# Kernel tuning notes

Measured on AMD Instinct MI355X. Metric: run time of the kernel, lower is better.

## Reference

```python
import jax, jax.numpy as jnp
import numpy as np

E = 8          # num_experts
TOP_K = 2      # router top-k
ALPHA = 1.702  # swigluoai alpha
LIMIT = 7.0    # swigluoai clamp limit


def setup_inputs() -> dict:
    key = jax.random.key(0)
    ks = jax.random.split(key, 7)
    B, S, H, I = 2, 1024, 1024, 1024
    s = 1.0 / np.sqrt(H)  # keep activations O(1), realistic init scale
    return {
        "x": jax.random.normal(ks[0], (B, S, H), jnp.float32),
        "router_weight": jax.random.normal(ks[1], (E, H), jnp.float32) * s,
        "router_bias": jax.random.normal(ks[2], (E,), jnp.float32) * 0.01,
        "w1": jax.random.normal(ks[3], (E, H, 2 * I), jnp.float32) * s,  # interleaved gate/up
        "w1_bias": jax.random.normal(ks[4], (E, 2 * I), jnp.float32) * 0.01,
        "w2": jax.random.normal(ks[5], (E, I, H), jnp.float32) * s,
        "w2_bias": jax.random.normal(ks[6], (E, H), jnp.float32) * 0.01,
    }


def _moe(x, router_weight, router_bias, w1, w1_bias, w2, w2_bias):
    B, S, H = x.shape
    xf = x.reshape(-1, H)                                   # [T, H]
    # ---- router: softmax over expert logits, then top-k ----
    logits = xf @ router_weight.T + router_bias             # [T, E]
    probs = jax.nn.softmax(logits, axis=-1)
    expert_weights, expert_ids = jax.lax.top_k(probs, TOP_K)  # [T, k]
    # combine weights scattered to dense [T, E] (no normalization: normalize_expert_weights=None)
    combine = jnp.sum(jax.nn.one_hot(expert_ids, E, dtype=xf.dtype)
                      * expert_weights[..., None], axis=1)  # [T, E]
    # ---- grouped MLP, expressed densely per expert (reference semantics) ----
    h = jnp.einsum('th,ehi->eti', xf, w1) + w1_bias[:, None, :]   # [E, T, 2I]
    gate = h[..., 0::2]                                          # interleaved layout
    up = h[..., 1::2]
    gate = jnp.minimum(gate, LIMIT)                              # swigluoai: clamp gate max
    up = jnp.clip(up, -LIMIT, LIMIT)                             # clamp up both sides
    glu = gate * jax.nn.sigmoid(gate * ALPHA)
    act = (up + 1.0) * glu                                       # [E, T, I]
    y = jnp.einsum('eti,eih->eth', act, w2) + w2_bias[:, None, :]  # [E, T, H]
    out = jnp.einsum('eth,te->th', y, combine)                   # weighted combine
    return out.reshape(B, S, H), expert_weights


def reference(x, router_weight, router_bias, w1, w1_bias, w2, w2_bias):
    return _moe(x, router_weight, router_bias, w1, w1_bias, w2, w2_bias)
```

## Files before the change

kernel.cpp:

```cpp
#include <hip/hip_runtime.h>
#include <cstdint>
#include <cstddef>

typedef unsigned short u16;
typedef short bf16x8 __attribute__((ext_vector_type(8)));
typedef float floatx4 __attribute__((ext_vector_type(4)));

#define GLD16(gp, sp) __builtin_amdgcn_global_load_lds(                      \
    (const __attribute__((address_space(1))) void*)(gp),                     \
    (__attribute__((address_space(3))) void*)(sp), 16, 0, 0)

#define VWAIT(N) asm volatile("s_waitcnt vmcnt(" #N ")" ::: "memory")
#define BARF()                                                               \
  do {                                                                       \
    __builtin_amdgcn_sched_barrier(0);                                       \
    __builtin_amdgcn_s_barrier();                                            \
    __builtin_amdgcn_sched_barrier(0);                                       \
  } while (0)

__device__ __forceinline__ u16 f2bf(float f) {
  unsigned u = __float_as_uint(f);
  u += 0x7fffu + ((u >> 16) & 1u);
  return (u16)(u >> 16);
}

__global__ void transpose_cvt_kernel(const float* __restrict__ in, u16* __restrict__ out,
                                     int R, int C) {
  __shared__ float tile[32][33];
  size_t base = (size_t)blockIdx.z * (size_t)R * (size_t)C;
  int c0 = blockIdx.x * 32, r0 = blockIdx.y * 32;
  int tx = threadIdx.x, ty = threadIdx.y;
#pragma unroll
  for (int k = 0; k < 32; k += 8)
    tile[ty + k][tx] = in[base + (size_t)(r0 + ty + k) * C + (c0 + tx)];
  __syncthreads();
#pragma unroll
  for (int k = 0; k < 32; k += 8)
    out[base + (size_t)(c0 + ty + k) * R + (r0 + tx)] = f2bf(tile[tx][ty + k]);
}

__global__ void router_kernel(const float* __restrict__ x, const float* __restrict__ rw,
                              const float* __restrict__ rb, float* __restrict__ ew,
                              int* __restrict__ eids, float* __restrict__ eprobs,
                              u16* __restrict__ xb) {
  const int wave = threadIdx.x >> 6, lane = threadIdx.x & 63;
  const int t = blockIdx.x * 4 + wave;
  const float4* xv = (const float4*)(x + (size_t)t * 1024);
  ushort4* xo = (ushort4*)(xb + (size_t)t * 1024);
  float acc[8];
#pragma unroll
  for (int e = 0; e < 8; ++e) acc[e] = 0.f;
  for (int j = lane; j < 256; j += 64) {
    float4 xx = xv[j];
    ushort4 o;
    o.x = f2bf(xx.x); o.y = f2bf(xx.y); o.z = f2bf(xx.z); o.w = f2bf(xx.w);
    xo[j] = o;
#pragma unroll
    for (int e = 0; e < 8; ++e) {
      float4 wv = ((const float4*)(rw + (size_t)e * 1024))[j];
      acc[e] += xx.x * wv.x + xx.y * wv.y + xx.z * wv.z + xx.w * wv.w;
    }
  }
#pragma unroll
  for (int e = 0; e < 8; ++e) {
    float v = acc[e];
#pragma unroll
    for (int off = 32; off > 0; off >>= 1) v += __shfl_down(v, off);
    acc[e] = v;
  }
  if (lane == 0) {
    float p[8];
    float mx = -1e30f;
#pragma unroll
    for (int e = 0; e < 8; ++e) { p[e] = acc[e] + rb[e]; mx = fmaxf(mx, p[e]); }
    float sum = 0.f;
#pragma unroll
    for (int e = 0; e < 8; ++e) { p[e] = __expf(p[e] - mx); sum += p[e]; }
    float inv = 1.f / sum;
#pragma unroll
    for (int e = 0; e < 8; ++e) p[e] *= inv;
    int i0 = 0;
#pragma unroll
    for (int e = 1; e < 8; ++e) if (p[e] > p[i0]) i0 = e;
    int i1 = (i0 == 0) ? 1 : 0;
#pragma unroll
    for (int e = 0; e < 8; ++e) if (e != i0 && e != i1 && p[e] > p[i1]) i1 = e;
    ew[t * 2 + 0] = p[i0];
    ew[t * 2 + 1] = p[i1];
    eids[t * 2 + 0] = i0;
    eids[t * 2 + 1] = i1;
    eprobs[t * 2 + 0] = p[i0];
    eprobs[t * 2 + 1] = p[i1];
  }
}

__global__ void build_lists_kernel(const int* __restrict__ eids, const float* __restrict__ eprobs,
                                   int* __restrict__ row_token, float* __restrict__ row_scale,
                                   int* __restrict__ tok2slot, int* __restrict__ meta) {
  __shared__ int cnt[8], base[8], cur[8];
  const int tid = threadIdx.x;
  if (tid < 8) { cnt[tid] = 0; cur[tid] = 0; }
  __syncthreads();
  for (int t = tid; t < 2048; t += 256) {
    atomicAdd(&cnt[eids[t * 2 + 0]], 1);
    atomicAdd(&cnt[eids[t * 2 + 1]], 1);
  }
  __syncthreads();
  if (tid == 0) {
    int off = 0, w = 0;
    for (int e = 0; e < 8; ++e) {
      base[e] = off;
      meta[48 + e] = off;
      int nb = (cnt[e] + 127) >> 7;
      for (int rb = 0; rb < nb; ++rb) meta[1 + w++] = (e << 8) | rb;
      off += nb << 7;
    }
    meta[0] = w;
  }
  __syncthreads();
  for (int s = tid; s < 5120; s += 256) { row_token[s] = -1; row_scale[s] = 0.f; }
  __syncthreads();
  for (int t = tid; t < 2048; t += 256) {
#pragma unroll
    for (int k = 0; k < 2; ++k) {
      int e = eids[t * 2 + k];
      int s = base[e] + atomicAdd(&cur[e], 1);
      row_token[s] = t;
      row_scale[s] = eprobs[t * 2 + k];
      tok2slot[t * 2 + k] = s;
    }
  }
}

__device__ __forceinline__ void g1_compute(const u16* AsR, const u16* BsR, int wr, int wc,
                                           int lane, floatx4 (&acc)[4][4]) {
  bf16x8 af[4], bfr[4];
#pragma unroll
  for (int mi = 0; mi < 4; ++mi) af[mi] = *(const bf16x8*)(AsR + (wr * 4 + mi) * 512 + lane * 8);
#pragma unroll
  for (int ni = 0; ni < 4; ++ni) bfr[ni] = *(const bf16x8*)(BsR + (wc * 4 + ni) * 512 + lane * 8);
  __builtin_amdgcn_s_setprio(1);
#pragma unroll
  for (int mi = 0; mi < 4; ++mi)
#pragma unroll
    for (int ni = 0; ni < 4; ++ni)
      acc[mi][ni] = __builtin_amdgcn_mfma_f32_16x16x32_bf16(af[mi], bfr[ni], acc[mi][ni], 0, 0, 0);
  __builtin_amdgcn_s_setprio(0);
}

__global__ __launch_bounds__(256) void gemm1_act_kernel(
    const u16* __restrict__ xb, const u16* __restrict__ w1t,
    const float* __restrict__ w1b,
    const int* __restrict__ row_token, const float* __restrict__ row_scale,
    const int* __restrict__ meta, u16* __restrict__ actS) {
  if ((int)blockIdx.x >= meta[0]) return;
  __shared__ __align__(16) u16 As[3][128 * 32];
  __shared__ __align__(16) u16 Bs[3][128 * 32];
  const int w = meta[1 + blockIdx.x];
  const int e = w >> 8, rb = w & 255;
  const int slotB = meta[48 + e] + rb * 128;
  const int colBase = blockIdx.y * 128;
  const int tid = threadIdx.x, lane = tid & 63, wave = tid >> 6;
  const int row16 = lane & 15, chunk = lane >> 4;
  const u16* Bt = w1t + (size_t)e * 2048 * 1024;
  const u16* aP[2]; const u16* bP[2];
#pragma unroll
  for (int r = 0; r < 2; ++r) {
    int g = r * 4 + wave;
    int tk = row_token[slotB + g * 16 + row16];
    if (tk < 0) tk = 0;
    aP[r] = xb + (size_t)tk * 1024 + chunk * 8;
    bP[r] = Bt + (size_t)(colBase + g * 16 + row16) * 1024 + chunk * 8;
  }
  const int wr = wave >> 1, wc = wave & 1;
  floatx4 acc[4][4];
#pragma unroll
  for (int mi = 0; mi < 4; ++mi)
#pragma unroll
    for (int ni = 0; ni < 4; ++ni) acc[mi][ni] = floatx4{0.f, 0.f, 0.f, 0.f};

#define G1_STAGE(W, KT)                                                      \
  {                                                                          \
    const int kk = (KT) * 32;                                                \
    GLD16(aP[0] + kk, As[W] + wave * 512);                                   \
    GLD16(bP[0] + kk, Bs[W] + wave * 512);                                   \
    GLD16(aP[1] + kk, As[W] + (4 + wave) * 512);                             \
    GLD16(bP[1] + kk, Bs[W] + (4 + wave) * 512);                             \
  }

  G1_STAGE(0, 0);
  G1_STAGE(1, 1);

#pragma unroll 1
  for (int kt = 0; kt < 30; kt += 3) {
    G1_STAGE(2, kt + 2); VWAIT(8); BARF();
    g1_compute(As[0], Bs[0], wr, wc, lane, acc); BARF();
    G1_STAGE(0, kt + 3); VWAIT(8); BARF();
    g1_compute(As[1], Bs[1], wr, wc, lane, acc); BARF();
    G1_STAGE(1, kt + 4); VWAIT(8); BARF();
    g1_compute(As[2], Bs[2], wr, wc, lane, acc); BARF();
  }
  VWAIT(4); BARF();
  g1_compute(As[0], Bs[0], wr, wc, lane, acc); BARF();
  VWAIT(0); BARF();
  g1_compute(As[1], Bs[1], wr, wc, lane, acc);
#undef G1_STAGE

  const int cl = lane & 15, ql = lane >> 4;
#pragma unroll
  for (int mi = 0; mi < 4; ++mi) {
#pragma unroll
    for (int r = 0; r < 4; ++r) {
      const int slot = slotB + wr * 64 + mi * 16 + ql * 4 + r;
      const float c = row_scale[slot];
#pragma unroll
      for (int ni = 0; ni < 4; ++ni) {
        const int n = colBase + wc * 64 + ni * 16 + cl;
        float v = acc[mi][ni][r] + w1b[e * 2048 + n];
        float o = __shfl_xor(v, 1);
        if ((lane & 1) == 0) {
          float g = fminf(v, 7.f);
          float u = fminf(fmaxf(o, -7.f), 7.f);
          float sg = 1.f / (1.f + __expf(-1.702f * g));
          float a = (u + 1.f) * (g * sg);
          actS[(size_t)slot * 1024 + (n >> 1)] = f2bf(c * a);
        }
      }
    }
  }
}

__device__ __forceinline__ void g2_compute(const u16* AsR, const u16* BsR, int wr, int wc,
                                           int lane, floatx4 (&acc)[4][2]) {
  bf16x8 af[4], bfr[2];
#pragma unroll
  for (int mi = 0; mi < 4; ++mi) af[mi] = *(const bf16x8*)(AsR + (wr * 4 + mi) * 512 + lane * 8);
#pragma unroll
  for (int ni = 0; ni < 2; ++ni) bfr[ni] = *(const bf16x8*)(BsR + (wc * 2 + ni) * 512 + lane * 8);
  __builtin_amdgcn_s_setprio(1);
#pragma unroll
  for (int mi = 0; mi < 4; ++mi)
#pragma unroll
    for (int ni = 0; ni < 2; ++ni)
      acc[mi][ni] = __builtin_amdgcn_mfma_f32_16x16x32_bf16(af[mi], bfr[ni], acc[mi][ni], 0, 0, 0);
  __builtin_amdgcn_s_setprio(0);
}

__global__ __launch_bounds__(256) void gemm2_kernel(
    const u16* __restrict__ actS, const u16* __restrict__ w2t,
    const int* __restrict__ meta, float* __restrict__ y) {
  if ((int)blockIdx.x >= meta[0]) return;
  __shared__ __align__(16) u16 As[3][128 * 32];
  __shared__ __align__(16) u16 Bs[3][64 * 32];
  const int w = meta[1 + blockIdx.x];
  const int e = w >> 8, rb = w & 255;
  const int slotB = meta[48 + e] + rb * 128;
  const int colBase = blockIdx.y * 64;
  const int tid = threadIdx.x, lane = tid & 63, wave = tid >> 6;
  const int row16 = lane & 15, chunk = lane >> 4;
  const u16* Bt = w2t + (size_t)e * 1024 * 1024;
  const u16* aP[2]; const u16* bP1;
#pragma unroll
  for (int r = 0; r < 2; ++r) {
    int g = r * 4 + wave;
    aP[r] = actS + (size_t)(slotB + g * 16 + row16) * 1024 + chunk * 8;
  }
  bP1 = Bt + (size_t)(colBase + wave * 16 + row16) * 1024 + chunk * 8;
  const int wr = wave >> 1, wc = wave & 1;
  floatx4 acc[4][2];
#pragma unroll
  for (int mi = 0; mi < 4; ++mi)
#pragma unroll
    for (int ni = 0; ni < 2; ++ni) acc[mi][ni] = floatx4{0.f, 0.f, 0.f, 0.f};

#define G2_STAGE(W, KT)                                                      \
  {                                                                          \
    const int kk = (KT) * 32;                                                \
    GLD16(aP[0] + kk, As[W] + wave * 512);                                   \
    GLD16(aP[1] + kk, As[W] + (4 + wave) * 512);                             \
    GLD16(bP1 + kk, Bs[W] + wave * 512);                                     \
  }

  G2_STAGE(0, 0);
  G2_STAGE(1, 1);

#pragma unroll 1
  for (int kt = 0; kt < 30; kt += 3) {
    G2_STAGE(2, kt + 2); VWAIT(6); BARF();
    g2_compute(As[0], Bs[0], wr, wc, lane, acc); BARF();
    G2_STAGE(0, kt + 3); VWAIT(6); BARF();
    g2_compute(As[1], Bs[1], wr, wc, lane, acc); BARF();
    G2_STAGE(1, kt + 4); VWAIT(6); BARF();
    g2_compute(As[2], Bs[2], wr, wc, lane, acc); BARF();
  }
  VWAIT(3); BARF();
  g2_compute(As[0], Bs[0], wr, wc, lane, acc); BARF();
  VWAIT(0); BARF();
  g2_compute(As[1], Bs[1], wr, wc, lane, acc);
#undef G2_STAGE

  const int cl = lane & 15, ql = lane >> 4;
#pragma unroll
  for (int mi = 0; mi < 4; ++mi)
#pragma unroll
    for (int r = 0; r < 4; ++r) {
      const int slot = slotB + wr * 64 + mi * 16 + ql * 4 + r;
#pragma unroll
      for (int ni = 0; ni < 2; ++ni) {
        const int col = colBase + wc * 32 + ni * 16 + cl;
        y[(size_t)slot * 1024 + col] = acc[mi][ni][r];
      }
    }
}

__global__ void combine_kernel(const float* __restrict__ y, const int* __restrict__ eids,
                               const float* __restrict__ eprobs, const int* __restrict__ tok2slot,
                               const float* __restrict__ w2b, float* __restrict__ out) {
  int idx = blockIdx.x * 256 + threadIdx.x;
  int t = idx >> 10, h = idx & 1023;
  int e0 = eids[t * 2], e1 = eids[t * 2 + 1];
  int s0 = tok2slot[t * 2], s1 = tok2slot[t * 2 + 1];
  out[idx] = eprobs[t * 2] * w2b[e0 * 1024 + h] + eprobs[t * 2 + 1] * w2b[e1 * 1024 + h]
           + y[(size_t)s0 * 1024 + h] + y[(size_t)s1 * 1024 + h];
}

extern "C" void kernel_launch(void* const* d_in, const int* in_sizes, int n_in,
                              void* d_out, int out_size, void* d_ws, size_t ws_size,
                              hipStream_t stream) {
  const float* x   = (const float*)d_in[0];
  const float* rw  = (const float*)d_in[1];
  const float* rb  = (const float*)d_in[2];
  const float* w1  = (const float*)d_in[3];
  const float* w1b = (const float*)d_in[4];
  const float* w2  = (const float*)d_in[5];
  const float* w2b = (const float*)d_in[6];
  float* out = (float*)d_out;
  float* ew  = out + (size_t)2048 * 1024;

  char* ws = (char*)d_ws;
  u16* xb        = (u16*)(ws);
  u16* w1t       = (u16*)(ws + (4ull << 20));
  float* y       = (float*)(ws + (4ull << 20));
  u16* w2t       = (u16*)(ws + (36ull << 20));
  u16* actS      = (u16*)(ws + (52ull << 20));
  int* eids      = (int*)(ws + (62ull << 20));
  float* eprobs  = (float*)(ws + (62ull << 20) + (16 << 10));
  int* row_token = (int*)(ws + (62ull << 20) + (32 << 10));
  float* row_scale = (float*)(ws + (62ull << 20) + (52 << 10));
  int* meta      = (int*)(ws + (62ull << 20) + (72 << 10));
  int* tok2slot  = (int*)(ws + (62ull << 20) + (74 << 10));

  transpose_cvt_kernel<<<dim3(64, 32, 8), dim3(32, 8), 0, stream>>>(w1, w1t, 1024, 2048);
  transpose_cvt_kernel<<<dim3(32, 32, 8), dim3(32, 8), 0, stream>>>(w2, w2t, 1024, 1024);
  router_kernel<<<512, 256, 0, stream>>>(x, rw, rb, ew, eids, eprobs, xb);
  build_lists_kernel<<<1, 256, 0, stream>>>(eids, eprobs, row_token, row_scale, tok2slot, meta);
  gemm1_act_kernel<<<dim3(40, 16), 256, 0, stream>>>(xb, w1t, w1b, row_token, row_scale, meta, actS);
  gemm2_kernel<<<dim3(40, 16), 256, 0, stream>>>(actS, w2t, meta, y);
  combine_kernel<<<8192, 256, 0, stream>>>(y, eids, eprobs, tok2slot, w2b, out);
}
```

Measured before the change: 262.5 us.

## Pre-gather routed token rows into contiguous bf16 buffer and merge weight transposes

Drops the bf16 conversion from the router and adds a gather kernel that writes each expert slot's token row, converted to bf16, into a contiguous buffer, so gemm1 reads A rows sequentially instead of through the row_token indirection. The two weight transpose launches are also merged into one grid, with early-exit blocks for the smaller w2 part. This costs an extra launch and about 10MB more write/read traffic for the gathered rows, and shifts the workspace offsets.

```diff
diff --git a/kernel.cpp b/kernel.cpp
--- a/kernel.cpp
+++ b/kernel.cpp
@@ -24,10 +24,15 @@
   return (u16)(u >> 16);
 }
 
-__global__ void transpose_cvt_kernel(const float* __restrict__ in, u16* __restrict__ out,
-                                     int R, int C) {
+__global__ void transpose_cvt2_kernel(const float* __restrict__ w1, u16* __restrict__ w1t,
+                                      const float* __restrict__ w2, u16* __restrict__ w2t) {
   __shared__ float tile[32][33];
-  size_t base = (size_t)blockIdx.z * (size_t)R * (size_t)C;
+  int z = blockIdx.z;
+  const float* in; u16* out; int C;
+  if (z < 8) { in = w1; out = w1t; C = 2048; }
+  else { if (blockIdx.x >= 32) return; in = w2; out = w2t; C = 1024; z -= 8; }
+  const int R = 1024;
+  size_t base = (size_t)z * (size_t)R * (size_t)C;
   int c0 = blockIdx.x * 32, r0 = blockIdx.y * 32;
   int tx = threadIdx.x, ty = threadIdx.y;
 #pragma unroll
@@ -41,20 +46,15 @@
 
 __global__ void router_kernel(const float* __restrict__ x, const float* __restrict__ rw,
                               const float* __restrict__ rb, float* __restrict__ ew,
-                              int* __restrict__ eids, float* __restrict__ eprobs,
-                              u16* __restrict__ xb) {
+                              int* __restrict__ eids, float* __restrict__ eprobs) {
   const int wave = threadIdx.x >> 6, lane = threadIdx.x & 63;
   const int t = blockIdx.x * 4 + wave;
   const float4* xv = (const float4*)(x + (size_t)t * 1024);
-  ushort4* xo = (ushort4*)(xb + (size_t)t * 1024);
   float acc[8];
 #pragma unroll
   for (int e = 0; e < 8; ++e) acc[e] = 0.f;
   for (int j = lane; j < 256; j += 64) {
     float4 xx = xv[j];
-    ushort4 o;
-    o.x = f2bf(xx.x); o.y = f2bf(xx.y); o.z = f2bf(xx.z); o.w = f2bf(xx.w);
-    xo[j] = o;
 #pragma unroll
     for (int e = 0; e < 8; ++e) {
       float4 wv = ((const float4*)(rw + (size_t)e * 1024))[j];
@@ -132,6 +132,20 @@
   }
 }
 
+__global__ void gather_x_kernel(const float* __restrict__ x, const int* __restrict__ row_token,
+                                u16* __restrict__ xg) {
+  const int s = blockIdx.x;
+  int tk = row_token[s];
+  if (tk < 0) tk = 0;
+  const float4* src = (const float4*)(x + (size_t)tk * 1024);
+  ushort4* dst = (ushort4*)(xg + (size_t)s * 1024);
+  const int t = threadIdx.x;
+  float4 v = src[t];
+  ushort4 o;
+  o.x = f2bf(v.x); o.y = f2bf(v.y); o.z = f2bf(v.z); o.w = f2bf(v.w);
+  dst[t] = o;
+}
+
 __device__ __forceinline__ void g1_compute(const u16* AsR, const u16* BsR, int wr, int wc,
                                            int lane, floatx4 (&acc)[4][4]) {
   bf16x8 af[4], bfr[4];
@@ -149,9 +163,8 @@
 }
 
 __global__ __launch_bounds__(256) void gemm1_act_kernel(
-    const u16* __restrict__ xb, const u16* __restrict__ w1t,
-    const float* __restrict__ w1b,
-    const int* __restrict__ row_token, const float* __restrict__ row_scale,
+    const u16* __restrict__ xg, const u16* __restrict__ w1t,
+    const float* __restrict__ w1b, const float* __restrict__ row_scale,
     const int* __restrict__ meta, u16* __restrict__ actS) {
   if ((int)blockIdx.x >= meta[0]) return;
   __shared__ __align__(16) u16 As[3][128 * 32];
@@ -167,9 +180,7 @@
 #pragma unroll
   for (int r = 0; r < 2; ++r) {
     int g = r * 4 + wave;
-    int tk = row_token[slotB + g * 16 + row16];
-    if (tk < 0) tk = 0;
-    aP[r] = xb + (size_t)tk * 1024 + chunk * 8;
+    aP[r] = xg + (size_t)(slotB + g * 16 + row16) * 1024 + chunk * 8;
     bP[r] = Bt + (size_t)(colBase + g * 16 + row16) * 1024 + chunk * 8;
   }
   const int wr = wave >> 1, wc = wave & 1;
@@ -338,23 +349,23 @@
   float* ew  = out + (size_t)2048 * 1024;
 
   char* ws = (char*)d_ws;
-  u16* xb        = (u16*)(ws);
-  u16* w1t       = (u16*)(ws + (4ull << 20));
-  float* y       = (float*)(ws + (4ull << 20));
-  u16* w2t       = (u16*)(ws + (36ull << 20));
-  u16* actS      = (u16*)(ws + (52ull << 20));
-  int* eids      = (int*)(ws + (62ull << 20));
-  float* eprobs  = (float*)(ws + (62ull << 20) + (16 << 10));
-  int* row_token = (int*)(ws + (62ull << 20) + (32 << 10));
-  float* row_scale = (float*)(ws + (62ull << 20) + (52 << 10));
-  int* meta      = (int*)(ws + (62ull << 20) + (72 << 10));
-  int* tok2slot  = (int*)(ws + (62ull << 20) + (74 << 10));
-
-  transpose_cvt_kernel<<<dim3(64, 32, 8), dim3(32, 8), 0, stream>>>(w1, w1t, 1024, 2048);
-  transpose_cvt_kernel<<<dim3(32, 32, 8), dim3(32, 8), 0, stream>>>(w2, w2t, 1024, 1024);
-  router_kernel<<<512, 256, 0, stream>>>(x, rw, rb, ew, eids, eprobs, xb);
+  u16* xg        = (u16*)(ws);
+  u16* w1t       = (u16*)(ws + (10ull << 20));
+  float* y       = (float*)(ws + (10ull << 20));
+  u16* w2t       = (u16*)(ws + (42ull << 20));
+  u16* actS      = (u16*)(ws + (58ull << 20));
+  int* eids      = (int*)(ws + (68ull << 20));
+  float* eprobs  = (float*)(ws + (68ull << 20) + (16 << 10));
+  int* row_token = (int*)(ws + (68ull << 20) + (32 << 10));
+  float* row_scale = (float*)(ws + (68ull << 20) + (52 << 10));
+  int* meta      = (int*)(ws + (68ull << 20) + (72 << 10));
+  int* tok2slot  = (int*)(ws + (68ull << 20) + (74 << 10));
+
+  transpose_cvt2_kernel<<<dim3(64, 32, 16), dim3(32, 8), 0, stream>>>(w1, w1t, w2, w2t);
+  router_kernel<<<512, 256, 0, stream>>>(x, rw, rb, ew, eids, eprobs);
   build_lists_kernel<<<1, 256, 0, stream>>>(eids, eprobs, row_token, row_scale, tok2slot, meta);
-  gemm1_act_kernel<<<dim3(40, 16), 256, 0, stream>>>(xb, w1t, w1b, row_token, row_scale, meta, actS);
+  gather_x_kernel<<<5120, 256, 0, stream>>>(x, row_token, xg);
+  gemm1_act_kernel<<<dim3(40, 16), 256, 0, stream>>>(xg, w1t, w1b, row_scale, meta, actS);
   gemm2_kernel<<<dim3(40, 16), 256, 0, stream>>>(actS, w2t, meta, y);
   combine_kernel<<<8192, 256, 0, stream>>>(y, eids, eprobs, tok2slot, w2b, out);
 }
```

Result: no change. 266.7 us (+1.6%).

## Fuse router and weight transposes into one kernel; widen gemm2 tile to 128 columns

Applied to the files above, without the earlier changes.

Merges the two weight transpose-convert kernels and the router into a single front_kernel, dispatched by block index, which removes two launches and lets the transposes overlap with router work. The transpose now uses 64x64 tiles with float4 loads and ushort4 stores for wider memory access. gemm2 now uses 128x128 tiles, reusing the gemm1 compute routine with a 4x4 accumulator, which halves the number of column blocks and doubles A-tile reuse. The trade is more registers and LDS per block and fewer blocks in flight.

```diff
diff --git a/kernel.cpp b/kernel.cpp
--- a/kernel.cpp
+++ b/kernel.cpp
@@ -24,27 +24,59 @@
   return (u16)(u >> 16);
 }
 
-__global__ void transpose_cvt_kernel(const float* __restrict__ in, u16* __restrict__ out,
-                                     int R, int C) {
-  __shared__ float tile[32][33];
-  size_t base = (size_t)blockIdx.z * (size_t)R * (size_t)C;
-  int c0 = blockIdx.x * 32, r0 = blockIdx.y * 32;
-  int tx = threadIdx.x, ty = threadIdx.y;
-#pragma unroll
-  for (int k = 0; k < 32; k += 8)
-    tile[ty + k][tx] = in[base + (size_t)(r0 + ty + k) * C + (c0 + tx)];
-  __syncthreads();
-#pragma unroll
-  for (int k = 0; k < 32; k += 8)
-    out[base + (size_t)(c0 + ty + k) * R + (r0 + tx)] = f2bf(tile[tx][ty + k]);
-}
-
-__global__ void router_kernel(const float* __restrict__ x, const float* __restrict__ rw,
-                              const float* __restrict__ rb, float* __restrict__ ew,
-                              int* __restrict__ eids, float* __restrict__ eprobs,
-                              u16* __restrict__ xb) {
+__device__ __forceinline__ void transpose64(const float* __restrict__ inb, u16* __restrict__ outb,
+                                            int C, int r0, int c0) {
+  __shared__ float tileT[64][65];
+  const int t = threadIdx.x;
+  const int k = t & 15, w = t >> 4;
+#pragma unroll
+  for (int it = 0; it < 4; ++it) {
+    const int r = r0 + w + it * 16;
+    const float4 v = *(const float4*)(inb + (size_t)r * C + (c0 + k * 4));
+    tileT[k * 4 + 0][w + it * 16] = v.x;
+    tileT[k * 4 + 1][w + it * 16] = v.y;
+    tileT[k * 4 + 2][w + it * 16] = v.z;
+    tileT[k * 4 + 3][w + it * 16] = v.w;
+  }
+  __syncthreads();
+#pragma unroll
+  for (int it = 0; it < 4; ++it) {
+    const int cc = w + it * 16;
+    const int r4 = k * 4;
+    ushort4 o;
+    o.x = f2bf(tileT[cc][r4 + 0]);
+    o.y = f2bf(tileT[cc][r4 + 1]);
+    o.z = f2bf(tileT[cc][r4 + 2]);
+    o.w = f2bf(tileT[cc][r4 + 3]);
+    *(ushort4*)(outb + (size_t)(c0 + cc) * 1024 + r0 + r4) = o;
+  }
+}
+
+__global__ __launch_bounds__(256) void front_kernel(
+    const float* __restrict__ x, const float* __restrict__ rw, const float* __restrict__ rb,
+    float* __restrict__ ew, int* __restrict__ eids, float* __restrict__ eprobs,
+    u16* __restrict__ xb,
+    const float* __restrict__ w1, u16* __restrict__ w1t,
+    const float* __restrict__ w2, u16* __restrict__ w2t) {
+  const int bid = blockIdx.x;
+  if (bid >= 512) {
+    int idx = bid - 512;
+    if (idx < 4096) {
+      const int e = idx >> 9, rem = idx & 511;
+      const int ct = rem & 31, rt = rem >> 5;
+      transpose64(w1 + (size_t)e * 1024 * 2048, w1t + (size_t)e * 2048 * 1024,
+                  2048, rt * 64, ct * 64);
+    } else {
+      idx -= 4096;
+      const int e = idx >> 8, rem = idx & 255;
+      const int ct = rem & 15, rt = rem >> 4;
+      transpose64(w2 + (size_t)e * 1024 * 1024, w2t + (size_t)e * 1024 * 1024,
+                  1024, rt * 64, ct * 64);
+    }
+    return;
+  }
   const int wave = threadIdx.x >> 6, lane = threadIdx.x & 63;
-  const int t = blockIdx.x * 4 + wave;
+  const int t = bid * 4 + wave;
   const float4* xv = (const float4*)(x + (size_t)t * 1024);
   ushort4* xo = (ushort4*)(xb + (size_t)t * 1024);
   float acc[8];
@@ -230,55 +262,40 @@
   }
 }
 
-__device__ __forceinline__ void g2_compute(const u16* AsR, const u16* BsR, int wr, int wc,
-                                           int lane, floatx4 (&acc)[4][2]) {
-  bf16x8 af[4], bfr[2];
-#pragma unroll
-  for (int mi = 0; mi < 4; ++mi) af[mi] = *(const bf16x8*)(AsR + (wr * 4 + mi) * 512 + lane * 8);
-#pragma unroll
-  for (int ni = 0; ni < 2; ++ni) bfr[ni] = *(const bf16x8*)(BsR + (wc * 2 + ni) * 512 + lane * 8);
-  __builtin_amdgcn_s_setprio(1);
-#pragma unroll
-  for (int mi = 0; mi < 4; ++mi)
-#pragma unroll
-    for (int ni = 0; ni < 2; ++ni)
-      acc[mi][ni] = __builtin_amdgcn_mfma_f32_16x16x32_bf16(af[mi], bfr[ni], acc[mi][ni], 0, 0, 0);
-  __builtin_amdgcn_s_setprio(0);
-}
-
 __global__ __launch_bounds__(256) void gemm2_kernel(
     const u16* __restrict__ actS, const u16* __restrict__ w2t,
     const int* __restrict__ meta, float* __restrict__ y) {
   if ((int)blockIdx.x >= meta[0]) return;
   __shared__ __align__(16) u16 As[3][128 * 32];
-  __shared__ __align__(16) u16 Bs[3][64 * 32];
+  __shared__ __align__(16) u16 Bs[3][128 * 32];
   const int w = meta[1 + blockIdx.x];
   const int e = w >> 8, rb = w & 255;
   const int slotB = meta[48 + e] + rb * 128;
-  const int colBase = blockIdx.y * 64;
+  const int colBase = blockIdx.y * 128;
   const int tid = threadIdx.x, lane = tid & 63, wave = tid >> 6;
   const int row16 = lane & 15, chunk = lane >> 4;
   const u16* Bt = w2t + (size_t)e * 1024 * 1024;
-  const u16* aP[2]; const u16* bP1;
+  const u16* aP[2]; const u16* bP[2];
 #pragma unroll
   for (int r = 0; r < 2; ++r) {
     int g = r * 4 + wave;
     aP[r] = actS + (size_t)(slotB + g * 16 + row16) * 1024 + chunk * 8;
-  }
-  bP1 = Bt + (size_t)(colBase + wave * 16 + row16) * 1024 + chunk * 8;
+    bP[r] = Bt + (size_t)(colBase + g * 16 + row16) * 1024 + chunk * 8;
+  }
   const int wr = wave >> 1, wc = wave & 1;
-  floatx4 acc[4][2];
+  floatx4 acc[4][4];
 #pragma unroll
   for (int mi = 0; mi < 4; ++mi)
 #pragma unroll
-    for (int ni = 0; ni < 2; ++ni) acc[mi][ni] = floatx4{0.f, 0.f, 0.f, 0.f};
+    for (int ni = 0; ni < 4; ++ni) acc[mi][ni] = floatx4{0.f, 0.f, 0.f, 0.f};
 
 #define G2_STAGE(W, KT)                                                      \
   {                                                                          \
     const int kk = (KT) * 32;                                                \
     GLD16(aP[0] + kk, As[W] + wave * 512);                                   \
+    GLD16(bP[0] + kk, Bs[W] + wave * 512);                                   \
     GLD16(aP[1] + kk, As[W] + (4 + wave) * 512);                             \
-    GLD16(bP1 + kk, Bs[W] + wave * 512);                                     \
+    GLD16(bP[1] + kk, Bs[W] + (4 + wave) * 512);                             \
   }
 
   G2_STAGE(0, 0);
@@ -286,17 +303,17 @@
 
 #pragma unroll 1
   for (int kt = 0; kt < 30; kt += 3) {
-    G2_STAGE(2, kt + 2); VWAIT(6); BARF();
-    g2_compute(As[0], Bs[0], wr, wc, lane, acc); BARF();
-    G2_STAGE(0, kt + 3); VWAIT(6); BARF();
-    g2_compute(As[1], Bs[1], wr, wc, lane, acc); BARF();
-    G2_STAGE(1, kt + 4); VWAIT(6); BARF();
-    g2_compute(As[2], Bs[2], wr, wc, lane, acc); BARF();
-  }
-  VWAIT(3); BARF();
-  g2_compute(As[0], Bs[0], wr, wc, lane, acc); BARF();
+    G2_STAGE(2, kt + 2); VWAIT(8); BARF();
+    g1_compute(As[0], Bs[0], wr, wc, lane, acc); BARF();
+    G2_STAGE(0, kt + 3); VWAIT(8); BARF();
+    g1_compute(As[1], Bs[1], wr, wc, lane, acc); BARF();
+    G2_STAGE(1, kt + 4); VWAIT(8); BARF();
+    g1_compute(As[2], Bs[2], wr, wc, lane, acc); BARF();
+  }
+  VWAIT(4); BARF();
+  g1_compute(As[0], Bs[0], wr, wc, lane, acc); BARF();
   VWAIT(0); BARF();
-  g2_compute(As[1], Bs[1], wr, wc, lane, acc);
+  g1_compute(As[1], Bs[1], wr, wc, lane, acc);
 #undef G2_STAGE
 
   const int cl = lane & 15, ql = lane >> 4;
@@ -306,8 +323,8 @@
     for (int r = 0; r < 4; ++r) {
       const int slot = slotB + wr * 64 + mi * 16 + ql * 4 + r;
 #pragma unroll
-      for (int ni = 0; ni < 2; ++ni) {
-        const int col = colBase + wc * 32 + ni * 16 + cl;
+      for (int ni = 0; ni < 4; ++ni) {
+        const int col = colBase + wc * 64 + ni * 16 + cl;
         y[(size_t)slot * 1024 + col] = acc[mi][ni][r];
       }
     }
@@ -350,11 +367,10 @@
   int* meta      = (int*)(ws + (62ull << 20) + (72 << 10));
   int* tok2slot  = (int*)(ws + (62ull << 20) + (74 << 10));
 
-  transpose_cvt_kernel<<<dim3(64, 32, 8), dim3(32, 8), 0, stream>>>(w1, w1t, 1024, 2048);
-  transpose_cvt_kernel<<<dim3(32, 32, 8), dim3(32, 8), 0, stream>>>(w2, w2t, 1024, 1024);
-  router_kernel<<<512, 256, 0, stream>>>(x, rw, rb, ew, eids, eprobs, xb);
+  front_kernel<<<512 + 4096 + 2048, 256, 0, stream>>>(x, rw, rb, ew, eids, eprobs, xb,
+                                                      w1, w1t, w2, w2t);
   build_lists_kernel<<<1, 256, 0, stream>>>(eids, eprobs, row_token, row_scale, tok2slot, meta);
   gemm1_act_kernel<<<dim3(40, 16), 256, 0, stream>>>(xb, w1t, w1b, row_token, row_scale, meta, actS);
-  gemm2_kernel<<<dim3(40, 16), 256, 0, stream>>>(actS, w2t, meta, y);
+  gemm2_kernel<<<dim3(40, 8), 256, 0, stream>>>(actS, w2t, meta, y);
   combine_kernel<<<8192, 256, 0, stream>>>(y, eids, eprobs, tok2slot, w2b, out);
 }
```

After: 250.5 us. 4.6% less time.
